# Optimization experiments

Hardware: AMD Instinct MI355X
Metric: run time of the kernel (lower is better)

The kernel has to match this reference:

```python
import jax, jax.numpy as jnp
import numpy as np

N, H_DIM, LATENT, MLP_H, F_OUT = 256, 128, 128, 256, 16
SUPP = 0.5  # ancestor_suppression_strength
EPS = 1e-12


def setup_inputs() -> dict:
    key = jax.random.key(0)
    ks = jax.random.split(key, 12)
    def w(k, shape):
        fan_in = shape[0]
        return jax.random.normal(k, shape, jnp.float32) / np.sqrt(fan_in)
    return {
        'z': jax.random.normal(ks[0], (LATENT,), jnp.float32),
        'targets': jax.random.randint(ks[1], (N, N), 0, 2, jnp.int32),
        'pos_emb': jax.random.normal(ks[2], (N, H_DIM), jnp.float32),
        'Ws1': w(ks[3], (H_DIM, H_DIM)),
        'Wn1': w(ks[4], (H_DIM, H_DIM)),
        'b1': jnp.zeros((H_DIM,), jnp.float32),
        'Ws2': w(ks[5], (H_DIM, H_DIM)),
        'Wn2': w(ks[6], (H_DIM, H_DIM)),
        'b2': jnp.zeros((H_DIM,), jnp.float32),
        'Wm1': w(ks[7], (LATENT + 3 * H_DIM, MLP_H)),
        'bm1': jnp.zeros((MLP_H,), jnp.float32),
        'Wm2': w(ks[8], (MLP_H, 1)),
        'bm2': jnp.zeros((1,), jnp.float32),
        'Wf': w(ks[9], (H_DIM, F_OUT)),
        'bf': jnp.zeros((F_OUT,), jnp.float32),
    }


def reference(z, targets, pos_emb, Ws1, Wn1, b1, Ws2, Wn2, b2,
              Wm1, bm1, Wm2, bm2, Wf, bf):
    tgt = jnp.tril(targets.astype(jnp.float32), -1)  # [N,N] strict lower: row=child, col=parent
    idx = jnp.arange(N)
    h0 = z  # decoder_init=None => hidden state init is z itself
    layers = ((Ws1, Wn1, b1), (Ws2, Wn2, b2))

    def gnn(Hs, M, active):
        # M[dst, src]: messages aggregated over incoming (parent) edges
        for Ws, Wn, b in layers:
            Hs = jax.nn.relu(Hs @ Ws + (M @ Hs) @ Wn + b) * active[:, None]
        return Hs

    def step(carry, t):
        Hs, anc, lp = carry
        Hs = Hs.at[t].set(h0 + pos_emb[t])          # new node t
        active = (idx <= t).astype(jnp.float32)
        M = tgt * (idx < t)[:, None].astype(jnp.float32)  # edges added in steps < t
        Hs = gnn(Hs, M, active)
        h_t = Hs[t]
        cand = (idx < t).astype(jnp.float32)        # candidate parents i < t
        mlp_in = jnp.concatenate([
            jnp.broadcast_to(h_t, (N, H_DIM)), Hs,
            jnp.broadcast_to(z, (N, LATENT)),
            jnp.broadcast_to(pos_emb[t], (N, H_DIM))], axis=1)
        logits = (jax.nn.relu(mlp_in @ Wm1 + bm1) @ Wm2 + bm2)[:, 0]
        probs = jax.nn.sigmoid(logits)
        # suppression[i] = prod_{j<t} (1 - s * anc[j][i])
        supp = jnp.prod(jnp.where((idx < t)[:, None], 1.0 - SUPP * anc, 1.0), axis=0)
        adj = probs * supp
        gt = tgt[t]
        logp = gt * jnp.log(adj + EPS) + (1.0 - gt) * jnp.log(1.0 - adj + EPS)
        lp = lp + jnp.sum(logp * cand)
        # ancestors of t = union over parents p of (anc[p] | {p})
        anc_t = jnp.minimum(1.0, gt @ anc + gt)
        anc = anc.at[t].set(anc_t)
        return (Hs, anc, lp), None

    H0 = jnp.zeros((N, H_DIM), jnp.float32).at[0].set(h0)
    anc0 = jnp.zeros((N, N), jnp.float32)
    (Hs, anc, lp), _ = jax.lax.scan(step, (H0, anc0, jnp.float32(0.0)), jnp.arange(1, N))
    # node_feature_decoder path: one more GNN pass over the full graph
    Hs = gnn(Hs, tgt, jnp.ones((N,), jnp.float32))
    X_out = Hs @ Wf + bf
    return tgt, X_out, lp
```

## Files before the change

kernel.cpp:

```cpp
#include <hip/hip_runtime.h>

#define NN 256
#define HD 128
#define GNN_NB 128
#define MLP_NB 64
#define NBLK 192
#define NTHR 512
#define D_HS 3
#define D_H1 2

#define HS_OFF 0
#define H1R_OFF 98304
#define PROG_OFF 163840
#define MF_OFF   (163840 + 4096)

#define STH_L 0
#define STM_L 256
#define PT_L  512
#define TGT_L 0
#define PTM_L 2048
#define PT3_L 10240
#define HC_L  11264
#define CT_L  11776
#define CZ_L  12032
#define W2_L  12288
#define HP_L  12544
#define PART_L 12800
#define ANC_L 13312
#define LP_L  13344
#define LDS_FLOATS 13360

__device__ __forceinline__ float2 ldc_f2(const float* p) {
    unsigned long long u = __hip_atomic_load((const unsigned long long*)p,
                                             __ATOMIC_RELAXED, __HIP_MEMORY_SCOPE_AGENT);
    float2 r;
    r.x = __uint_as_float((unsigned)u);
    r.y = __uint_as_float((unsigned)(u >> 32));
    return r;
}
__device__ __forceinline__ void stc_f(float* p, float v) {
    __hip_atomic_store((unsigned*)p, __float_as_uint(v),
                       __ATOMIC_RELAXED, __HIP_MEMORY_SCOPE_AGENT);
}
__device__ __forceinline__ unsigned ldf(const unsigned* p) {
    return __hip_atomic_load(p, __ATOMIC_RELAXED, __HIP_MEMORY_SCOPE_AGENT);
}
__device__ __forceinline__ void stf(unsigned* p, unsigned v) {
    __hip_atomic_store(p, v, __ATOMIC_RELAXED, __HIP_MEMORY_SCOPE_AGENT);
}

__device__ __forceinline__ void bar_lds() {
    asm volatile("s_waitcnt lgkmcnt(0)\n\ts_barrier" ::: "memory");
}

#define ISS(i) \
    float2 va##i, vb##i, vc##i, vd##i; \
    if ((i) < nst) { \
        const float* p_ = gsrc + (i) * 32 * HD; \
        if ((un >> (4 * (i)    )) & 1u) va##i = ldc_f2(p_); \
        if ((un >> (4 * (i) + 1)) & 1u) vb##i = ldc_f2(p_ + HD); \
        if ((un >> (4 * (i) + 2)) & 1u) vc##i = ldc_f2(p_ + 2 * HD); \
        if ((un >> (4 * (i) + 3)) & 1u) vd##i = ldc_f2(p_ + 3 * HD); \
    }
#define ACCP(v, b) { \
    const float f0_ = (float)((s0 >> (b)) & 1u); \
    const float f1_ = (float)((s1 >> (b)) & 1u); \
    m0.x = fmaf(f0_, v.x, m0.x); m0.y = fmaf(f0_, v.y, m0.y); \
    m1.x = fmaf(f1_, v.x, m1.x); m1.y = fmaf(f1_, v.y, m1.y); }
#define ACC1(v, b) if ((un >> (b)) & 1u) { ACCP(v, b) }
#define CNS(i) if ((i) < nst) { ACC1(va##i, 4*(i)) ACC1(vb##i, 4*(i)+1) \
                                ACC1(vc##i, 4*(i)+2) ACC1(vd##i, 4*(i)+3) }

__device__ __forceinline__ void layer(const float* src, float* dst, float bc,
    const float* z, const float* pos_emb, float* lds,
    const float (&wsA)[32], const float (&wnA)[32],
    unsigned mk0, unsigned mk1,
    int R0, int rmax, int tgate, int tnew, int lane, int wv, int tid, int c, int kbase)
{
    const int rmaxblk = min(rmax, R0 + 1);
    const int nst = (rmaxblk + 31) >> 5;
    const unsigned s0 = (R0     < tgate) ? mk0 : 0u;
    const unsigned s1 = (R0 + 1 < tgate) ? mk1 : 0u;
    const unsigned un = s0 | s1;

    if (tnew >= R0 && tnew < R0 + 2) {
        const int dr = tnew - R0;
        if (tid < HD) lds[STH_L + dr * HD + tid] = z[tid] + pos_emb[tnew * HD + tid];
    }

    const float* gsrc = src + wv * 4 * HD + 2 * lane;
    float2 m0 = make_float2(0.f, 0.f), m1 = m0;
    ISS(0) ISS(1) ISS(2) ISS(3) ISS(4) ISS(5) ISS(6) ISS(7)
    CNS(0) CNS(1) CNS(2) CNS(3) CNS(4) CNS(5) CNS(6) CNS(7)

    float* pt = lds + PT_L + (wv * 2) * HD + 2 * lane;
    *(float2*)pt = m0;
    *(float2*)(pt + HD) = m1;
    bar_lds();
    if (tid < 256) {
        const int dr = tid >> 7, k = tid & 127;
        float s = 0.f;
#pragma unroll
        for (int w = 0; w < 8; ++w) s += lds[PT_L + (w * 2 + dr) * HD + k];
        lds[STM_L + dr * HD + k] = s;
    }
    bar_lds();
    float acc0 = 0.f, acc1 = 0.f;
#pragma unroll
    for (int q = 0; q < 8; ++q) {
        const float4 h0 = *(const float4*)(lds + STH_L + kbase + 4 * q);
        const float4 mm0 = *(const float4*)(lds + STM_L + kbase + 4 * q);
        const float4 h1 = *(const float4*)(lds + STH_L + HD + kbase + 4 * q);
        const float4 mm1 = *(const float4*)(lds + STM_L + HD + kbase + 4 * q);
        acc0 = fmaf(h0.x, wsA[4*q],   fmaf(mm0.x, wnA[4*q],   acc0));
        acc0 = fmaf(h0.y, wsA[4*q+1], fmaf(mm0.y, wnA[4*q+1], acc0));
        acc0 = fmaf(h0.z, wsA[4*q+2], fmaf(mm0.z, wnA[4*q+2], acc0));
        acc0 = fmaf(h0.w, wsA[4*q+3], fmaf(mm0.w, wnA[4*q+3], acc0));
        acc1 = fmaf(h1.x, wsA[4*q],   fmaf(mm1.x, wnA[4*q],   acc1));
        acc1 = fmaf(h1.y, wsA[4*q+1], fmaf(mm1.y, wnA[4*q+1], acc1));
        acc1 = fmaf(h1.z, wsA[4*q+2], fmaf(mm1.z, wnA[4*q+2], acc1));
        acc1 = fmaf(h1.w, wsA[4*q+3], fmaf(mm1.w, wnA[4*q+3], acc1));
    }
    acc0 += __shfl_xor(acc0, 16); acc0 += __shfl_xor(acc0, 32);
    acc1 += __shfl_xor(acc1, 16); acc1 += __shfl_xor(acc1, 32);
    const float o0 = fmaxf(acc0 + bc, 0.f);
    const float o1 = fmaxf(acc1 + bc, 0.f);
    const int kg = lane >> 4;
    if (kg == 0) { if (R0     <= rmaxblk) stc_f(dst + R0 * HD + c, o0); }
    else if (kg == 1) { if (R0 + 1 <= rmaxblk) stc_f(dst + (R0 + 1) * HD + c, o1); }
    else if (kg == 2) lds[STH_L + c] = o0;
    else              lds[STH_L + HD + c] = o1;
}

__device__ __forceinline__ void ct_calc(const float* hsP, const float* pos_emb,
                                        const float* Wm1, float* lds, int s)
{
    const int tid = threadIdx.x;
    if (tid < 64) {
        const float2 v = ldc_f2(hsP + s * HD + 2 * tid);
        lds[HP_L + 2 * tid] = v.x; lds[HP_L + 2 * tid + 1] = v.y;
    } else if (tid < 128) {
        const int l2 = tid - 64;
        lds[HP_L + 128 + 2 * l2]     = pos_emb[s * HD + 2 * l2];
        lds[HP_L + 128 + 2 * l2 + 1] = pos_emb[s * HD + 2 * l2 + 1];
    }
    __syncthreads();
    const int c = tid & 255, half = tid >> 8;
    float acc = 0.f;
    const float* w = half ? (Wm1 + 384 * 256 + c) : (Wm1 + c);
    const float* hh = lds + HP_L + half * 128;
#pragma unroll 4
    for (int k = 0; k < HD; ++k) acc = fmaf(hh[k], w[k * 256], acc);
    lds[PART_L + half * 256 + c] = acc;
    __syncthreads();
    if (tid < 256)
        lds[CT_L + tid] = lds[CZ_L + tid] + lds[PART_L + tid] + lds[PART_L + 256 + tid];
}

__device__ __forceinline__ void mlp_step(const float* hsP, const float* bm2,
                                         const float4 (&wm)[16], float* lds, int mb, int s)
{
    const int tid = threadIdx.x, lane = tid & 63, wv = tid >> 6;
    const int ks = wv * 16;
    if (wv < 4) {
        const int i = 4 * mb + wv;
        float2 v = make_float2(0.f, 0.f);
        if (i < s) v = ldc_f2(hsP + i * HD + 2 * lane);
        *(float2*)(lds + HC_L + wv * HD + 2 * lane) = v;
    }
    __syncthreads();
    float4 a0 = make_float4(0.f, 0.f, 0.f, 0.f), a1 = a0, a2 = a0, a3 = a0;
#pragma unroll
    for (int kk = 0; kk < 16; ++kk) {
        const int k = ks + kk;
        const float h0 = lds[HC_L + 0 * HD + k];
        const float h1 = lds[HC_L + 1 * HD + k];
        const float h2 = lds[HC_L + 2 * HD + k];
        const float h3 = lds[HC_L + 3 * HD + k];
        const float4 w = wm[kk];
        a0.x = fmaf(h0, w.x, a0.x); a0.y = fmaf(h0, w.y, a0.y);
        a0.z = fmaf(h0, w.z, a0.z); a0.w = fmaf(h0, w.w, a0.w);
        a1.x = fmaf(h1, w.x, a1.x); a1.y = fmaf(h1, w.y, a1.y);
        a1.z = fmaf(h1, w.z, a1.z); a1.w = fmaf(h1, w.w, a1.w);
        a2.x = fmaf(h2, w.x, a2.x); a2.y = fmaf(h2, w.y, a2.y);
        a2.z = fmaf(h2, w.z, a2.z); a2.w = fmaf(h2, w.w, a2.w);
        a3.x = fmaf(h3, w.x, a3.x); a3.y = fmaf(h3, w.y, a3.y);
        a3.z = fmaf(h3, w.z, a3.z); a3.w = fmaf(h3, w.w, a3.w);
    }
    *(float4*)(lds + PTM_L + (wv * 4 + 0) * 256 + 4 * lane) = a0;
    *(float4*)(lds + PTM_L + (wv * 4 + 1) * 256 + 4 * lane) = a1;
    *(float4*)(lds + PTM_L + (wv * 4 + 2) * 256 + 4 * lane) = a2;
    *(float4*)(lds + PTM_L + (wv * 4 + 3) * 256 + 4 * lane) = a3;
    __syncthreads();
    {
        const int c = tid & 255, ci2 = (tid >> 8) * 2;
#pragma unroll
        for (int q = 0; q < 2; ++q) {
            const int ci = ci2 + q;
            float v = lds[CT_L + c];
#pragma unroll
            for (int w = 0; w < 8; ++w) v += lds[PTM_L + (w * 4 + ci) * 256 + c];
            lds[PT3_L + ci * 256 + c] = fmaxf(v, 0.f) * lds[W2_L + c];
        }
    }
    __syncthreads();
    if (wv < 4) {
        const int ci = wv, i = 4 * mb + ci;
        if (i < s) {
            float sd = lds[PT3_L + ci * 256 + lane] + lds[PT3_L + ci * 256 + 64 + lane]
                     + lds[PT3_L + ci * 256 + 128 + lane] + lds[PT3_L + ci * 256 + 192 + lane];
#pragma unroll
            for (int off = 32; off > 0; off >>= 1) sd += __shfl_xor(sd, off);
            if (lane == 0) {
                const unsigned* gtl = (const unsigned*)(lds + TGT_L) + s * 8;
                unsigned* ancl = (unsigned*)(lds + ANC_L);
                const float logit = sd + bm2[0];
                const float prob = 1.f / (1.f + expf(-logit));
                unsigned cnt = 0, has = 0;
#pragma unroll
                for (int w = 0; w < 8; ++w) {
                    const unsigned av = ancl[ci * 8 + w];
                    cnt += __popc(av);
                    has |= av & gtl[w];
                }
                const float supp = ldexpf(1.f, -(int)cnt);
                const float adj = prob * supp;
                const unsigned gt = (gtl[i >> 5] >> (i & 31)) & 1u;
                const float lpv = gt ? logf(adj + 1e-12f) : logf(1.f - adj + 1e-12f);
                atomicAdd((float*)(lds + LP_L), lpv);
                if (has | gt) ancl[ci * 8 + (s >> 5)] |= (1u << (s & 31));
            }
        }
    }
}

extern "C" __global__ void __launch_bounds__(NTHR)
fused_gnn(const float* z, const int* targets, const float* pos_emb,
          const float* Ws1, const float* Wn1, const float* b1,
          const float* Ws2, const float* Wn2, const float* b2,
          const float* Wm1, const float* bm1, const float* Wm2, const float* bm2,
          const float* Wf, const float* bf, float* out, float* ws)
{
    __shared__ __align__(16) float lds[LDS_FLOATS];
    const int b = blockIdx.x;
    const int tid = threadIdx.x, lane = tid & 63, wv = tid >> 6;

    unsigned* prog = (unsigned*)(ws + PROG_OFF);
    unsigned* mf   = (unsigned*)(ws + MF_OFF);
    float* lp_out = out + NN * NN + NN * 16;

    if (b < GNN_NB) {
        const int R0 = b * 2;
        const int c = 16 * wv + (lane & 15);
        const int kbase = 32 * (lane >> 4);
        float ws1[32], wn1[32], ws2[32], wn2[32];
#pragma unroll
        for (int i = 0; i < 32; ++i) {
            ws1[i] = Ws1[(kbase + i) * HD + c];
            wn1[i] = Wn1[(kbase + i) * HD + c];
            ws2[i] = Ws2[(kbase + i) * HD + c];
            wn2[i] = Wn2[(kbase + i) * HD + c];
        }
        const float b1c = b1[c], b2c = b2[c];
        unsigned mk0, mk1;
        {
            const int srcl = (lane < 32) ? (((lane >> 2) << 5) + wv * 4 + (lane & 3)) : 0;
#define BALLOT_MK(dr, dst) { \
            const int r_ = R0 + (dr); \
            const bool p_ = (lane < 32) && (srcl < r_) && (targets[r_ * NN + srcl] != 0); \
            const unsigned long long bm_ = __ballot(p_); \
            dst = (unsigned)__builtin_amdgcn_readfirstlane((int)(unsigned)bm_); }
            BALLOT_MK(0, mk0) BALLOT_MK(1, mk1)
#undef BALLOT_MK
        }
        if (tid < 256) lds[STH_L + tid] = (b == 0 && tid < HD) ? z[tid] : 0.f;
        if (tid < 256) {
            const int dr = tid >> 7, cc = tid & 127, r = R0 + dr;
            stc_f(ws + HS_OFF + r * HD + cc, (r == 0) ? z[cc] : 0.f);
        }
        if (wv < 2) {
            const int r = R0 + wv;
            const int4 tv = ((const int4*)(targets + r * NN))[lane];
            float4 ov;
            ov.x = (4 * lane     < r) ? (float)tv.x : 0.f;
            ov.y = (4 * lane + 1 < r) ? (float)tv.y : 0.f;
            ov.z = (4 * lane + 2 < r) ? (float)tv.z : 0.f;
            ov.w = (4 * lane + 3 < r) ? (float)tv.w : 0.f;
            ((float4*)(out + r * NN))[lane] = ov;
        }
        __syncthreads();
        if (tid == 0) stf(prog + b * 32, 1u);

        unsigned seenP = 0;
        int      seenM = 0;

        for (int t = 1; t <= 256; ++t) {
            const float* hsP = ws + HS_OFF + ((t - 1) % D_HS) * 32768;
            float* h1c = ws + H1R_OFF + (t & 1) * 32768;
            float* hsN = ws + HS_OFF + (t % D_HS) * 32768;
            const int rmax  = (t <= 255) ? t : 255;
            const int tgate = (t <= 255) ? t : 300;
            const int tnew  = (t <= 255) ? t : -1;
            const bool act = (R0 <= rmax);

            if (act) {
                {
                    const unsigned dataTh = 2u * t - 1u;
                    const unsigned ringTh = (t > D_H1) ? (2u * (t - D_H1) + 1u) : 0u;
                    if (tid < GNN_NB) {
                        const unsigned th = (tid < b) ? dataTh : ringTh;
                        if (seenP < th) {
                            unsigned v;
                            for (;;) {
                                v = ldf(prog + tid * 32);
                                if (v >= th) break;
                                __builtin_amdgcn_s_sleep(1);
                            }
                            seenP = v;
                        }
                    }
                    __syncthreads();
                    asm volatile("" ::: "memory");
                }
                layer(hsP, h1c, b1c, z, pos_emb, lds, ws1, wn1,
                      mk0, mk1, R0, rmax, tgate, tnew, lane, wv, tid, c, kbase);
            }
            __syncthreads();
            if (tid == 0) stf(prog + b * 32, 2u * t);

            if (act) {
                {
                    const unsigned dataTh = 2u * t;
                    const unsigned ringTh = (t > D_HS) ? (2u * (t - D_HS + 1)) : 0u;
                    const int mlpTh = t - D_HS;
                    const bool ownRow = (mlpTh > 0) && ((mlpTh >> 1) == b);
                    if (tid < GNN_NB) {
                        const unsigned th = (tid < b) ? dataTh : ringTh;
                        if (seenP < th) {
                            unsigned v;
                            for (;;) {
                                v = ldf(prog + tid * 32);
                                if (v >= th) break;
                                __builtin_amdgcn_s_sleep(1);
                            }
                            seenP = v;
                        }
                    } else if (tid < GNN_NB + MLP_NB) {
                        const int mi = tid - GNN_NB;
                        const int thm = (mlpTh > 0 && (mi == (b >> 1) || ownRow)) ? mlpTh : 0;
                        if (thm > 0 && seenM < thm) {
                            int v;
                            for (;;) {
                                v = (int)ldf(mf + mi * 32);
                                if (v >= thm) break;
                                __builtin_amdgcn_s_sleep(1);
                            }
                            seenM = v;
                        }
                    }
                    __syncthreads();
                    asm volatile("" ::: "memory");
                }
                layer(h1c, hsN, b2c, z, pos_emb, lds, ws2, wn2,
                      mk0, mk1, R0, rmax, tgate, -1, lane, wv, tid, c, kbase);
            }
            __syncthreads();
            if (tid == 0) stf(prog + b * 32, 2u * t + 1u);
        }

        if (wv < 2) {
            const int r = R0 + wv;
            const float* strow = lds + STH_L + wv * HD;
            const int f = lane & 15, kp = lane >> 4;
            float sacc = 0.f;
#pragma unroll
            for (int k = 0; k < 32; ++k)
                sacc = fmaf(strow[kp * 32 + k], Wf[(kp * 32 + k) * 16 + f], sacc);
            sacc += __shfl_xor(sacc, 16);
            sacc += __shfl_xor(sacc, 32);
            if (lane < 16) out[NN * NN + r * 16 + f] = sacc + bf[f];
        }
    } else {
        const int mb = b - GNN_NB;
        const int ks = wv * 16;
        float4 wm[16];
#pragma unroll
        for (int kk = 0; kk < 16; ++kk)
            wm[kk] = *(const float4*)(Wm1 + (128 + ks + kk) * 256 + 4 * lane);
        {
            unsigned* tg = (unsigned*)(lds + TGT_L);
            for (int rr = 0; rr < 32; ++rr) {
                const int r = wv * 32 + rr;
#pragma unroll
                for (int q = 0; q < 4; ++q) {
                    const int j = q * 64 + lane;
                    const unsigned long long bm = __ballot(j < r && targets[r * NN + j] != 0);
                    if (lane == 0) {
                        tg[r * 8 + 2 * q]     = (unsigned)bm;
                        tg[r * 8 + 2 * q + 1] = (unsigned)(bm >> 32);
                    }
                }
            }
        }
        if (tid < 256) {
            lds[W2_L + tid] = Wm2[tid];
            float acc = bm1[tid];
            for (int k = 0; k < HD; ++k) acc = fmaf(z[k], Wm1[(256 + k) * 256 + tid], acc);
            lds[CZ_L + tid] = acc;
        }
        if (tid < 32) ((unsigned*)(lds + ANC_L))[tid] = 0u;
        if (tid == 0) lds[LP_L] = 0.f;

        unsigned seenP = 0;
        for (int s = 1; s <= 255; ++s) {
            if (4 * mb < s && tid < GNN_NB) {
                const bool needed = (tid == 2 * mb) || (tid == 2 * mb + 1) ||
                                    (tid == (s >> 1));
                if (needed) {
                    const unsigned need = 2u * (unsigned)s + 1u;
                    if (seenP < need) {
                        unsigned v;
                        for (;;) {
                            v = ldf(prog + tid * 32);
                            if (v >= need) break;
                            __builtin_amdgcn_s_sleep(1);
                        }
                        seenP = v;
                    }
                }
            }
            __syncthreads();
            const float* hsP = ws + HS_OFF + (s % D_HS) * 32768;
            if (4 * mb < s) {
                ct_calc(hsP, pos_emb, Wm1, lds, s);
                __syncthreads();
                mlp_step(hsP, bm2, wm, lds, mb, s);
            }
            __syncthreads();
            if (tid == 0) stf(mf + mb * 32, (unsigned)s);
        }
        __syncthreads();
        if (tid == 0) atomicAdd(lp_out, lds[LP_L]);
    }
}

extern "C" void kernel_launch(void* const* d_in, const int* in_sizes, int n_in,
                              void* d_out, int out_size, void* d_ws, size_t ws_size,
                              hipStream_t stream)
{
    const float* z       = (const float*)d_in[0];
    const int*   targets = (const int*)d_in[1];
    const float* pos_emb = (const float*)d_in[2];
    const float* Ws1     = (const float*)d_in[3];
    const float* Wn1     = (const float*)d_in[4];
    const float* b1      = (const float*)d_in[5];
    const float* Ws2     = (const float*)d_in[6];
    const float* Wn2     = (const float*)d_in[7];
    const float* b2      = (const float*)d_in[8];
    const float* Wm1     = (const float*)d_in[9];
    const float* bm1     = (const float*)d_in[10];
    const float* Wm2     = (const float*)d_in[11];
    const float* bm2     = (const float*)d_in[12];
    const float* Wf      = (const float*)d_in[13];
    const float* bf      = (const float*)d_in[14];
    float* out = (float*)d_out;
    float* ws  = (float*)d_ws;

    (void)hipMemsetAsync(ws + PROG_OFF, 0, (GNN_NB + MLP_NB) * 32 * sizeof(unsigned), stream);
    (void)hipMemsetAsync(out + NN * NN + NN * 16, 0, sizeof(float), stream);

    void* args[17] = {
        (void*)&z, (void*)&targets, (void*)&pos_emb,
        (void*)&Ws1, (void*)&Wn1, (void*)&b1,
        (void*)&Ws2, (void*)&Wn2, (void*)&b2,
        (void*)&Wm1, (void*)&bm1, (void*)&Wm2, (void*)&bm2,
        (void*)&Wf, (void*)&bf, (void*)&out, (void*)&ws
    };
    (void)hipLaunchCooperativeKernel((const void*)fused_gnn, dim3(NBLK), dim3(NTHR),
                                     args, 0, stream);
}
```

Baseline: 1.798 ms.

## Replace progress-flag data waits with step-tagged 64-bit values in hidden-state rings

Each hidden-state element is now stored as a 64-bit word that packs the float value with the step tag it was written at. Consumers spin on the tag of the data they read instead of waiting on per-block progress flags. This removes most of the flag polling in the GNN layers and all of it in the MLP blocks, leaving only ring-reuse waits. The cost is doubled memory traffic for hidden states and more complex spin loops on the data itself.

```diff
diff --git a/kernel.cpp b/kernel.cpp
--- a/kernel.cpp
+++ b/kernel.cpp
@@ -1,4 +1,6 @@
 #include <hip/hip_runtime.h>
+
+typedef unsigned long long u64;
 
 #define NN 256
 #define HD 128
@@ -6,13 +8,10 @@
 #define MLP_NB 64
 #define NBLK 192
 #define NTHR 512
-#define D_HS 3
-#define D_H1 2
-
-#define HS_OFF 0
-#define H1R_OFF 98304
-#define PROG_OFF 163840
-#define MF_OFF   (163840 + 4096)
+
+#define HS_U 0
+#define H1_U 98304
+#define FLAG_BYTE 1310720
 
 #define STH_L 0
 #define STM_L 256
@@ -30,18 +29,17 @@
 #define LP_L  13344
 #define LDS_FLOATS 13360
 
-__device__ __forceinline__ float2 ldc_f2(const float* p) {
-    unsigned long long u = __hip_atomic_load((const unsigned long long*)p,
-                                             __ATOMIC_RELAXED, __HIP_MEMORY_SCOPE_AGENT);
-    float2 r;
-    r.x = __uint_as_float((unsigned)u);
-    r.y = __uint_as_float((unsigned)(u >> 32));
-    return r;
-}
-__device__ __forceinline__ void stc_f(float* p, float v) {
-    __hip_atomic_store((unsigned*)p, __float_as_uint(v),
-                       __ATOMIC_RELAXED, __HIP_MEMORY_SCOPE_AGENT);
-}
+__device__ __forceinline__ u64 ldp(const u64* p) {
+    return __hip_atomic_load(p, __ATOMIC_RELAXED, __HIP_MEMORY_SCOPE_AGENT);
+}
+__device__ __forceinline__ void stp(u64* p, u64 v) {
+    __hip_atomic_store(p, v, __ATOMIC_RELAXED, __HIP_MEMORY_SCOPE_AGENT);
+}
+__device__ __forceinline__ u64 pk(float v, unsigned tg) {
+    return ((u64)tg << 32) | (u64)__float_as_uint(v);
+}
+#define VALF(v) __uint_as_float((unsigned)(v))
+#define TAGU(v) ((unsigned)((v) >> 32))
 __device__ __forceinline__ unsigned ldf(const unsigned* p) {
     return __hip_atomic_load(p, __ATOMIC_RELAXED, __HIP_MEMORY_SCOPE_AGENT);
 }
@@ -54,25 +52,33 @@
 }
 
 #define ISS(i) \
-    float2 va##i, vb##i, vc##i, vd##i; \
+    u64 va##i, wa##i, vb##i, wb##i, vc##i, wc##i, vd##i, wd##i; \
     if ((i) < nst) { \
-        const float* p_ = gsrc + (i) * 32 * HD; \
-        if ((un >> (4 * (i)    )) & 1u) va##i = ldc_f2(p_); \
-        if ((un >> (4 * (i) + 1)) & 1u) vb##i = ldc_f2(p_ + HD); \
-        if ((un >> (4 * (i) + 2)) & 1u) vc##i = ldc_f2(p_ + 2 * HD); \
-        if ((un >> (4 * (i) + 3)) & 1u) vd##i = ldc_f2(p_ + 3 * HD); \
-    }
-#define ACCP(v, b) { \
+        const u64* p_ = gsrc + (i) * 32 * HD; \
+        if ((un >> (4*(i)  )) & 1u) { va##i = ldp(p_);          wa##i = ldp(p_ + 1); } \
+        if ((un >> (4*(i)+1)) & 1u) { vb##i = ldp(p_ + HD);     wb##i = ldp(p_ + HD + 1); } \
+        if ((un >> (4*(i)+2)) & 1u) { vc##i = ldp(p_ + 2*HD);   wc##i = ldp(p_ + 2*HD + 1); } \
+        if ((un >> (4*(i)+3)) & 1u) { vd##i = ldp(p_ + 3*HD);   wd##i = ldp(p_ + 3*HD + 1); } \
+    }
+#define ACCP2(v, w, b) { \
     const float f0_ = (float)((s0 >> (b)) & 1u); \
     const float f1_ = (float)((s1 >> (b)) & 1u); \
-    m0.x = fmaf(f0_, v.x, m0.x); m0.y = fmaf(f0_, v.y, m0.y); \
-    m1.x = fmaf(f1_, v.x, m1.x); m1.y = fmaf(f1_, v.y, m1.y); }
-#define ACC1(v, b) if ((un >> (b)) & 1u) { ACCP(v, b) }
-#define CNS(i) if ((i) < nst) { ACC1(va##i, 4*(i)) ACC1(vb##i, 4*(i)+1) \
-                                ACC1(vc##i, 4*(i)+2) ACC1(vd##i, 4*(i)+3) }
-
-__device__ __forceinline__ void layer(const float* src, float* dst, float bc,
-    const float* z, const float* pos_emb, float* lds,
+    const float x_ = VALF(v), y_ = VALF(w); \
+    m0.x = fmaf(f0_, x_, m0.x); m0.y = fmaf(f0_, y_, m0.y); \
+    m1.x = fmaf(f1_, x_, m1.x); m1.y = fmaf(f1_, y_, m1.y); }
+#define ACC1(v, w, b, po) \
+    if ((un >> (b)) & 1u) { \
+        while (__builtin_expect(TAGU(v) != etag || TAGU(w) != etag, 0)) { \
+            v = ldp(po); w = ldp((po) + 1); } \
+        ACCP2(v, w, b) }
+#define CNS(i) if ((i) < nst) { \
+    ACC1(va##i, wa##i, 4*(i),   gsrc + (i)*32*HD) \
+    ACC1(vb##i, wb##i, 4*(i)+1, gsrc + (i)*32*HD + HD) \
+    ACC1(vc##i, wc##i, 4*(i)+2, gsrc + (i)*32*HD + 2*HD) \
+    ACC1(vd##i, wd##i, 4*(i)+3, gsrc + (i)*32*HD + 3*HD) }
+
+__device__ __forceinline__ void layer(const u64* src, u64* dst, unsigned etag, unsigned wtag,
+    float bc, const float* z, const float* pos_emb, float* lds,
     const float (&wsA)[32], const float (&wnA)[32],
     unsigned mk0, unsigned mk1,
     int R0, int rmax, int tgate, int tnew, int lane, int wv, int tid, int c, int kbase)
@@ -88,7 +94,7 @@
         if (tid < HD) lds[STH_L + dr * HD + tid] = z[tid] + pos_emb[tnew * HD + tid];
     }
 
-    const float* gsrc = src + wv * 4 * HD + 2 * lane;
+    const u64* gsrc = src + wv * 4 * HD + 2 * lane;
     float2 m0 = make_float2(0.f, 0.f), m1 = m0;
     ISS(0) ISS(1) ISS(2) ISS(3) ISS(4) ISS(5) ISS(6) ISS(7)
     CNS(0) CNS(1) CNS(2) CNS(3) CNS(4) CNS(5) CNS(6) CNS(7)
@@ -126,19 +132,22 @@
     const float o0 = fmaxf(acc0 + bc, 0.f);
     const float o1 = fmaxf(acc1 + bc, 0.f);
     const int kg = lane >> 4;
-    if (kg == 0) { if (R0     <= rmaxblk) stc_f(dst + R0 * HD + c, o0); }
-    else if (kg == 1) { if (R0 + 1 <= rmaxblk) stc_f(dst + (R0 + 1) * HD + c, o1); }
+    if (kg == 0) { if (R0     <= rmaxblk) stp(dst + R0 * HD + c, pk(o0, wtag)); }
+    else if (kg == 1) { if (R0 + 1 <= rmaxblk) stp(dst + (R0 + 1) * HD + c, pk(o1, wtag)); }
     else if (kg == 2) lds[STH_L + c] = o0;
     else              lds[STH_L + HD + c] = o1;
 }
 
-__device__ __forceinline__ void ct_calc(const float* hsP, const float* pos_emb,
+__device__ __forceinline__ void ct_calc(const u64* hsP, const float* pos_emb,
                                         const float* Wm1, float* lds, int s)
 {
     const int tid = threadIdx.x;
     if (tid < 64) {
-        const float2 v = ldc_f2(hsP + s * HD + 2 * tid);
-        lds[HP_L + 2 * tid] = v.x; lds[HP_L + 2 * tid + 1] = v.y;
+        const u64* p = hsP + s * HD + 2 * tid;
+        u64 a = ldp(p), b2 = ldp(p + 1);
+        const unsigned e = (unsigned)s;
+        while (__builtin_expect(TAGU(a) != e || TAGU(b2) != e, 0)) { a = ldp(p); b2 = ldp(p + 1); }
+        lds[HP_L + 2 * tid] = VALF(a); lds[HP_L + 2 * tid + 1] = VALF(b2);
     } else if (tid < 128) {
         const int l2 = tid - 64;
         lds[HP_L + 128 + 2 * l2]     = pos_emb[s * HD + 2 * l2];
@@ -157,16 +166,23 @@
         lds[CT_L + tid] = lds[CZ_L + tid] + lds[PART_L + tid] + lds[PART_L + 256 + tid];
 }
 
-__device__ __forceinline__ void mlp_step(const float* hsP, const float* bm2,
+__device__ __forceinline__ void mlp_step(const u64* hsP, const float* bm2,
                                          const float4 (&wm)[16], float* lds, int mb, int s)
 {
     const int tid = threadIdx.x, lane = tid & 63, wv = tid >> 6;
     const int ks = wv * 16;
     if (wv < 4) {
         const int i = 4 * mb + wv;
-        float2 v = make_float2(0.f, 0.f);
-        if (i < s) v = ldc_f2(hsP + i * HD + 2 * lane);
-        *(float2*)(lds + HC_L + wv * HD + 2 * lane) = v;
+        float vx = 0.f, vy = 0.f;
+        if (i < s) {
+            const u64* p = hsP + i * HD + 2 * lane;
+            u64 a = ldp(p), b2 = ldp(p + 1);
+            const unsigned e = (unsigned)s;
+            while (__builtin_expect(TAGU(a) != e || TAGU(b2) != e, 0)) { a = ldp(p); b2 = ldp(p + 1); }
+            vx = VALF(a); vy = VALF(b2);
+        }
+        lds[HC_L + wv * HD + 2 * lane] = vx;
+        lds[HC_L + wv * HD + 2 * lane + 1] = vy;
     }
     __syncthreads();
     float4 a0 = make_float4(0.f, 0.f, 0.f, 0.f), a1 = a0, a2 = a0, a3 = a0;
@@ -245,8 +261,11 @@
     const int b = blockIdx.x;
     const int tid = threadIdx.x, lane = tid & 63, wv = tid >> 6;
 
-    unsigned* prog = (unsigned*)(ws + PROG_OFF);
-    unsigned* mf   = (unsigned*)(ws + MF_OFF);
+    u64* wsu = (u64*)ws;
+    u64* hsRing = wsu + HS_U;
+    u64* h1Ring = wsu + H1_U;
+    unsigned* prog = (unsigned*)((char*)ws + FLAG_BYTE);
+    unsigned* mf = prog + 128 * 32;
     float* lp_out = out + NN * NN + NN * 16;
 
     if (b < GNN_NB) {
@@ -276,7 +295,7 @@
         if (tid < 256) lds[STH_L + tid] = (b == 0 && tid < HD) ? z[tid] : 0.f;
         if (tid < 256) {
             const int dr = tid >> 7, cc = tid & 127, r = R0 + dr;
-            stc_f(ws + HS_OFF + r * HD + cc, (r == 0) ? z[cc] : 0.f);
+            stp(hsRing + r * HD + cc, pk((r == 0) ? z[cc] : 0.f, 0u));
         }
         if (wv < 2) {
             const int r = R0 + wv;
@@ -295,52 +314,46 @@
         int      seenM = 0;
 
         for (int t = 1; t <= 256; ++t) {
-            const float* hsP = ws + HS_OFF + ((t - 1) % D_HS) * 32768;
-            float* h1c = ws + H1R_OFF + (t & 1) * 32768;
-            float* hsN = ws + HS_OFF + (t % D_HS) * 32768;
+            const u64* hsP = hsRing + ((t - 1) % 3) * 32768;
+            u64* h1c = h1Ring + (t & 1) * 32768;
+            u64* hsN = hsRing + (t % 3) * 32768;
             const int rmax  = (t <= 255) ? t : 255;
             const int tgate = (t <= 255) ? t : 300;
             const int tnew  = (t <= 255) ? t : -1;
             const bool act = (R0 <= rmax);
 
             if (act) {
+                if (t > 2 && tid < GNN_NB) {
+                    const unsigned th = 2u * (t - 2) + 1u;
+                    if (seenP < th) {
+                        unsigned v;
+                        for (;;) {
+                            v = ldf(prog + tid * 32);
+                            if (v >= th) break;
+                            __builtin_amdgcn_s_sleep(1);
+                        }
+                        seenP = v;
+                    }
+                }
+                __syncthreads();
+                asm volatile("" ::: "memory");
+                layer(hsP, h1c, (unsigned)(t - 1), (unsigned)t, b1c, z, pos_emb, lds,
+                      ws1, wn1, mk0, mk1, R0, rmax, tgate, tnew, lane, wv, tid, c, kbase);
+            }
+            __syncthreads();
+            if (tid == 0) stf(prog + b * 32, 2u * t);
+
+            if (act) {
                 {
-                    const unsigned dataTh = 2u * t - 1u;
-                    const unsigned ringTh = (t > D_H1) ? (2u * (t - D_H1) + 1u) : 0u;
+                    const unsigned ringTh = (t > 3) ? (2u * (t - 2)) : 0u;
+                    const int mlpTh = t - 3;
+                    const bool ownRow = (mlpTh > 0) && ((mlpTh >> 1) == b);
                     if (tid < GNN_NB) {
-                        const unsigned th = (tid < b) ? dataTh : ringTh;
-                        if (seenP < th) {
+                        if (ringTh && seenP < ringTh) {
                             unsigned v;
                             for (;;) {
                                 v = ldf(prog + tid * 32);
-                                if (v >= th) break;
-                                __builtin_amdgcn_s_sleep(1);
-                            }
-                            seenP = v;
-                        }
-                    }
-                    __syncthreads();
-                    asm volatile("" ::: "memory");
-                }
-                layer(hsP, h1c, b1c, z, pos_emb, lds, ws1, wn1,
-                      mk0, mk1, R0, rmax, tgate, tnew, lane, wv, tid, c, kbase);
-            }
-            __syncthreads();
-            if (tid == 0) stf(prog + b * 32, 2u * t);
-
-            if (act) {
-                {
-                    const unsigned dataTh = 2u * t;
-                    const unsigned ringTh = (t > D_HS) ? (2u * (t - D_HS + 1)) : 0u;
-                    const int mlpTh = t - D_HS;
-                    const bool ownRow = (mlpTh > 0) && ((mlpTh >> 1) == b);
-                    if (tid < GNN_NB) {
-                        const unsigned th = (tid < b) ? dataTh : ringTh;
-                        if (seenP < th) {
-                            unsigned v;
-                            for (;;) {
-                                v = ldf(prog + tid * 32);
-                                if (v >= th) break;
+                                if (v >= ringTh) break;
                                 __builtin_amdgcn_s_sleep(1);
                             }
                             seenP = v;
@@ -361,8 +374,8 @@
                     __syncthreads();
                     asm volatile("" ::: "memory");
                 }
-                layer(h1c, hsN, b2c, z, pos_emb, lds, ws2, wn2,
-                      mk0, mk1, R0, rmax, tgate, -1, lane, wv, tid, c, kbase);
+                layer(h1c, hsN, (unsigned)t, (unsigned)t, b2c, z, pos_emb, lds,
+                      ws2, wn2, mk0, mk1, R0, rmax, tgate, -1, lane, wv, tid, c, kbase);
             }
             __syncthreads();
             if (tid == 0) stf(prog + b * 32, 2u * t + 1u);
@@ -410,27 +423,10 @@
         }
         if (tid < 32) ((unsigned*)(lds + ANC_L))[tid] = 0u;
         if (tid == 0) lds[LP_L] = 0.f;
-
-        unsigned seenP = 0;
+        __syncthreads();
+
         for (int s = 1; s <= 255; ++s) {
-            if (4 * mb < s && tid < GNN_NB) {
-                const bool needed = (tid == 2 * mb) || (tid == 2 * mb + 1) ||
-                                    (tid == (s >> 1));
-                if (needed) {
-                    const unsigned need = 2u * (unsigned)s + 1u;
-                    if (seenP < need) {
-                        unsigned v;
-                        for (;;) {
-                            v = ldf(prog + tid * 32);
-                            if (v >= need) break;
-                            __builtin_amdgcn_s_sleep(1);
-                        }
-                        seenP = v;
-                    }
-                }
-            }
-            __syncthreads();
-            const float* hsP = ws + HS_OFF + (s % D_HS) * 32768;
+            const u64* hsP = hsRing + (s % 3) * 32768;
             if (4 * mb < s) {
                 ct_calc(hsP, pos_emb, Wm1, lds, s);
                 __syncthreads();
@@ -466,7 +462,7 @@
     float* out = (float*)d_out;
     float* ws  = (float*)d_ws;
 
-    (void)hipMemsetAsync(ws + PROG_OFF, 0, (GNN_NB + MLP_NB) * 32 * sizeof(unsigned), stream);
+    (void)hipMemsetAsync((char*)d_ws + FLAG_BYTE, 0, (128 + 64) * 32 * sizeof(unsigned), stream);
     (void)hipMemsetAsync(out + NN * NN + NN * 16, 0, sizeof(float), stream);
 
     void* args[17] = {
```

Result: slower. 2.752 ms (+53.1%).
